# Kernel optimization log

Measured on AMD Instinct MI355X. Metric: run time of the kernel, lower is better.

Reference implementation:

```python
import jax, jax.numpy as jnp
import numpy as np
from jax import lax


def setup_inputs() -> dict:
    key = jax.random.key(0)
    k1, k2 = jax.random.split(key)
    C, H, W = 64, 224, 224
    C_out, hf, wf = 128, 3, 3
    x = jax.random.normal(k1, (C, H, W), dtype=jnp.float32)
    kernels = jax.random.normal(k2, (C_out, C, hf, wf), dtype=jnp.float32)
    return {"x": x, "kernels": kernels}


def reference(x, kernels):
    # Original builds im2col columns per output pixel then does k_col @ x_col,
    # i.e. a cross-correlation with 'valid' padding and stride 1.
    # lax.conv_general_dilated computes exactly this (no kernel flip).
    stride = 1
    out = lax.conv_general_dilated(
        x[None],                       # (1, C, H, W) NCHW
        kernels,                       # (C_out, C_in, hf, wf) OIHW
        window_strides=(stride, stride),
        padding="VALID",
        dimension_numbers=("NCHW", "OIHW", "NCHW"),
    )
    return out[0]                      # (C_out, H_out, W_out)
```

## Files before the change

kernel.cpp:

```cpp
#include <hip/hip_runtime.h>
#include <hip/hip_bf16.h>


#define H_IN   224
#define W_IN   224
#define C_OUT  128
#define H_OUT  222
#define W_OUT  222
#define XP     226
#define TW     68

typedef __attribute__((ext_vector_type(8)))  short bf16x8;
typedef __attribute__((ext_vector_type(16))) float f32x16;

static __device__ __forceinline__ unsigned short f2bs(float f) {
    union { __hip_bfloat16 h; unsigned short u; } cv;
    cv.h = __float2bfloat16(f);
    return cv.u;
}

__global__ __launch_bounds__(256)
void transform_w_kernel(const float* __restrict__ w, __hip_bfloat16* __restrict__ wt)
{
    int idx = blockIdx.x * 256 + threadIdx.x;
    if (idx < 9 * 128 * 64) {
        int ij  = idx >> 13;
        int rem = idx & 8191;
        int co  = rem >> 6;
        int c   = rem & 63;
        wt[((ij * 8 + (c >> 3)) * 128 + co) * 8 + (c & 7)] =
            __float2bfloat16(w[(co * 64 + c) * 9 + ij]);
    }
}

__global__ __launch_bounds__(256)
void transpose_x_kernel(const float* __restrict__ x, __hip_bfloat16* __restrict__ xt)
{
    __shared__ __align__(16) unsigned short tile[64 * TW];
    const int h  = blockIdx.y;
    const int w0 = blockIdx.x * 64;
    const int t  = threadIdx.x;

    {
        const int wq = (t & 15) * 4;
        const int c0 = t >> 4;
        #pragma unroll
        for (int p = 0; p < 4; ++p) {
            const int c  = c0 + p * 16;
            const int wg = w0 + wq;
            float4 v = make_float4(0.f, 0.f, 0.f, 0.f);
            if (h < H_IN && wg < W_IN)
                v = *(const float4*)(x + ((size_t)c * H_IN + h) * W_IN + wg);
            ushort4 b;
            b.x = f2bs(v.x); b.y = f2bs(v.y); b.z = f2bs(v.z); b.w = f2bs(v.w);
            *(ushort4*)(tile + c * TW + wq) = b;
        }
    }
    __syncthreads();

    {
        const int wl = t >> 2;
        const int cq = (t & 3) * 16;
        const int wg = w0 + wl;
        if (wg < XP) {
            alignas(16) unsigned short r[16];
            #pragma unroll
            for (int k = 0; k < 16; ++k)
                r[k] = tile[(cq + k) * TW + wl];
            float4* d = (float4*)((unsigned short*)xt + ((size_t)h * XP + wg) * 64 + cq);
            d[0] = ((const float4*)r)[0];
            d[1] = ((const float4*)r)[1];
        }
    }
}

__global__ __launch_bounds__(256)
void conv_mfma_kernel(const __hip_bfloat16* __restrict__ xt,
                      const __hip_bfloat16* __restrict__ wt,
                      float* __restrict__ out)
{
    __shared__ __hip_bfloat16 xs[10 * 34 * 64];
    const int ow0 = blockIdx.x * 32;
    const int oh0 = blockIdx.y * 8;
    const int co0 = blockIdx.z * 64;
    const int tid = threadIdx.x;

    for (int q = tid; q < 10 * 34 * 8; q += 256) {
        int sub = q & 7;
        int pix = q >> 3;
        int row = pix / 34;
        int wc  = pix - row * 34;
        int chunk = sub ^ (wc & 3);
        *(float4*)(xs + pix * 64 + chunk * 8) =
            *(const float4*)(xt + ((oh0 + row) * XP + (ow0 + wc)) * 64 + sub * 8);
    }
    __syncthreads();

    const int wave = tid >> 6;
    const int lane = tid & 63;
    const int n    = lane & 31;
    const int h    = lane >> 5;
    const int r0   = wave * 2;

    f32x16 acc[2][2] = {};

    #pragma unroll
    for (int p = 0; p < 9; ++p) {
        const int i  = p / 3;
        const int jj = p - i * 3;

        bf16x8 afr[4][2];
        #pragma unroll
        for (int t = 0; t < 4; ++t)
            #pragma unroll
            for (int mi = 0; mi < 2; ++mi)
                afr[t][mi] = *(const bf16x8*)(wt +
                    ((p * 8 + t * 2 + h) * 128 + co0 + mi * 32 + n) * 8);

        #pragma unroll
        for (int t = 0; t < 4; ++t) {
            bf16x8 bfr[2];
            #pragma unroll
            for (int ni = 0; ni < 2; ++ni) {
                const int wc    = n + jj;
                const int pix   = (i + r0 + ni) * 34 + wc;
                const int chunk = (t * 2 + h) ^ (wc & 3);
                bfr[ni] = *(const bf16x8*)(xs + pix * 64 + chunk * 8);
            }
            #pragma unroll
            for (int mi = 0; mi < 2; ++mi)
                #pragma unroll
                for (int ni = 0; ni < 2; ++ni)
                    acc[mi][ni] = __builtin_amdgcn_mfma_f32_32x32x16_bf16(
                        afr[t][mi], bfr[ni], acc[mi][ni], 0, 0, 0);
        }
    }

    #pragma unroll
    for (int mi = 0; mi < 2; ++mi) {
        #pragma unroll
        for (int ni = 0; ni < 2; ++ni) {
            const int oh = oh0 + r0 + ni;
            const int ow = ow0 + n;
            if (oh < H_OUT && ow < W_OUT) {
                #pragma unroll
                for (int r = 0; r < 16; ++r) {
                    int co = co0 + mi * 32 + (r & 3) + 8 * (r >> 2) + 4 * h;
                    out[(size_t)co * (H_OUT * W_OUT) + oh * W_OUT + ow] = acc[mi][ni][r];
                }
            }
        }
    }
}

extern "C" void kernel_launch(void* const* d_in, const int* in_sizes, int n_in,
                              void* d_out, int out_size, void* d_ws, size_t ws_size,
                              hipStream_t stream)
{
    const float* x = (const float*)d_in[0];
    const float* w = (const float*)d_in[1];
    float* out     = (float*)d_out;

    __hip_bfloat16* xt = (__hip_bfloat16*)d_ws;
    __hip_bfloat16* wt = (__hip_bfloat16*)((char*)d_ws + (size_t)XP * XP * 64 * 2);

    transform_w_kernel<<<288, 256, 0, stream>>>(w, wt);
    transpose_x_kernel<<<dim3(4, XP), 256, 0, stream>>>(x, xt);
    conv_mfma_kernel<<<dim3(7, 28, 2), 256, 0, stream>>>(xt, wt, out);
}
```

Measured before the change: 91.93 us.

## Store input in channel-chunk-major layout and read MFMA B operands directly from global

Changes the transposed input layout from pixel-major with 64 contiguous channels to [row][channel-chunk][column] float4 units. With this layout, adjacent lanes load adjacent 16-byte chunks. The conv kernel drops its shared-memory staging tile and barrier and loads B fragments straight from global/L2 inside the 9-tap loop. This removes LDS traffic and the sync, but every B fragment is now re-read from cache across the taps, waves and output-channel blocks, so the kernel leans on L1/L2 hit rates and load latency.

```diff
diff --git a/kernel.cpp b/kernel.cpp
--- a/kernel.cpp
+++ b/kernel.cpp
@@ -34,7 +34,7 @@
 }
 
 __global__ __launch_bounds__(256)
-void transpose_x_kernel(const float* __restrict__ x, __hip_bfloat16* __restrict__ xt)
+void transpose_x_kernel(const float* __restrict__ x, float4* __restrict__ xt4)
 {
     __shared__ __align__(16) unsigned short tile[64 * TW];
     const int h  = blockIdx.y;
@@ -61,40 +61,28 @@
     {
         const int wl = t >> 2;
         const int cq = (t & 3) * 16;
+        const int ch = (t & 3) * 2;
         const int wg = w0 + wl;
         if (wg < XP) {
             alignas(16) unsigned short r[16];
             #pragma unroll
             for (int k = 0; k < 16; ++k)
                 r[k] = tile[(cq + k) * TW + wl];
-            float4* d = (float4*)((unsigned short*)xt + ((size_t)h * XP + wg) * 64 + cq);
-            d[0] = ((const float4*)r)[0];
-            d[1] = ((const float4*)r)[1];
+            xt4[((size_t)h * 8 + ch)     * XP + wg] = ((const float4*)r)[0];
+            xt4[((size_t)h * 8 + ch + 1) * XP + wg] = ((const float4*)r)[1];
         }
     }
 }
 
 __global__ __launch_bounds__(256)
-void conv_mfma_kernel(const __hip_bfloat16* __restrict__ xt,
+void conv_mfma_kernel(const float4* __restrict__ xt4,
                       const __hip_bfloat16* __restrict__ wt,
                       float* __restrict__ out)
 {
-    __shared__ __hip_bfloat16 xs[10 * 34 * 64];
     const int ow0 = blockIdx.x * 32;
     const int oh0 = blockIdx.y * 8;
     const int co0 = blockIdx.z * 64;
     const int tid = threadIdx.x;
-
-    for (int q = tid; q < 10 * 34 * 8; q += 256) {
-        int sub = q & 7;
-        int pix = q >> 3;
-        int row = pix / 34;
-        int wc  = pix - row * 34;
-        int chunk = sub ^ (wc & 3);
-        *(float4*)(xs + pix * 64 + chunk * 8) =
-            *(const float4*)(xt + ((oh0 + row) * XP + (ow0 + wc)) * 64 + sub * 8);
-    }
-    __syncthreads();
 
     const int wave = tid >> 6;
     const int lane = tid & 63;
@@ -110,30 +98,30 @@
         const int jj = p - i * 3;
 
         bf16x8 afr[4][2];
+        bf16x8 bfr[4][2];
         #pragma unroll
-        for (int t = 0; t < 4; ++t)
+        for (int t = 0; t < 4; ++t) {
             #pragma unroll
             for (int mi = 0; mi < 2; ++mi)
                 afr[t][mi] = *(const bf16x8*)(wt +
                     ((p * 8 + t * 2 + h) * 128 + co0 + mi * 32 + n) * 8);
+            #pragma unroll
+            for (int ni = 0; ni < 2; ++ni) {
+                const int row = oh0 + r0 + ni + i;
+                const int ch  = t * 2 + h;
+                bfr[t][ni] = *(const bf16x8*)(xt4 +
+                    ((size_t)row * 8 + ch) * XP + ow0 + n + jj);
+            }
+        }
 
         #pragma unroll
-        for (int t = 0; t < 4; ++t) {
-            bf16x8 bfr[2];
-            #pragma unroll
-            for (int ni = 0; ni < 2; ++ni) {
-                const int wc    = n + jj;
-                const int pix   = (i + r0 + ni) * 34 + wc;
-                const int chunk = (t * 2 + h) ^ (wc & 3);
-                bfr[ni] = *(const bf16x8*)(xs + pix * 64 + chunk * 8);
-            }
+        for (int t = 0; t < 4; ++t)
             #pragma unroll
             for (int mi = 0; mi < 2; ++mi)
                 #pragma unroll
                 for (int ni = 0; ni < 2; ++ni)
                     acc[mi][ni] = __builtin_amdgcn_mfma_f32_32x32x16_bf16(
-                        afr[t][mi], bfr[ni], acc[mi][ni], 0, 0, 0);
-        }
+                        afr[t][mi], bfr[t][ni], acc[mi][ni], 0, 0, 0);
     }
 
     #pragma unroll
@@ -161,10 +149,10 @@
     const float* w = (const float*)d_in[1];
     float* out     = (float*)d_out;
 
-    __hip_bfloat16* xt = (__hip_bfloat16*)d_ws;
+    float4* xt4        = (float4*)d_ws;
     __hip_bfloat16* wt = (__hip_bfloat16*)((char*)d_ws + (size_t)XP * XP * 64 * 2);
 
     transform_w_kernel<<<288, 256, 0, stream>>>(w, wt);
-    transpose_x_kernel<<<dim3(4, XP), 256, 0, stream>>>(x, xt);
-    conv_mfma_kernel<<<dim3(7, 28, 2), 256, 0, stream>>>(xt, wt, out);
+    transpose_x_kernel<<<dim3(4, XP), 256, 0, stream>>>(x, xt4);
+    conv_mfma_kernel<<<dim3(7, 28, 2), 256, 0, stream>>>(xt4, wt, out);
 }
```

Result: no change. 90.68 us (-1.4%).
